# Kernel optimization log

Hardware: AMD Instinct MI355X
Metric: run time of the kernel (lower is better)

## Reference

```python
import jax, jax.numpy as jnp
import numpy as np

VOCAB, T, IN, H, L = 32000, 4096, 512, 256, 2


def setup_inputs() -> dict:
    key = jax.random.key(0)
    ks = jax.random.split(key, 32)
    inp = {}
    inp["tokens"] = jax.random.randint(ks[0], (T,), 0, VOCAB)
    inp["emb"] = jax.random.normal(ks[1], (VOCAB, IN), dtype=jnp.float32) * 0.02
    i = 2
    for d in ("f", "b"):
        for l in range(L):
            in_l = IN if l == 0 else H
            inp[f"{d}_Wih{l}"] = jax.random.normal(ks[i], (4 * H, in_l), dtype=jnp.float32) * 0.05; i += 1
            inp[f"{d}_Whh{l}"] = jax.random.normal(ks[i], (4 * H, H), dtype=jnp.float32) * 0.05; i += 1
            inp[f"{d}_bih{l}"] = jnp.zeros((4 * H,), dtype=jnp.float32)
            inp[f"{d}_bhh{l}"] = jnp.zeros((4 * H,), dtype=jnp.float32)
    return inp


def _lstm_layer(x_seq, Wih, Whh, bih, bhh):
    # x_seq: [T, in]; torch.nn.LSTMCell gate order: i, f, g, o
    Hh = Whh.shape[1]
    b = bih + bhh
    def step(carry, x):
        h, c = carry
        g = x @ Wih.T + h @ Whh.T + b           # [4H]
        i_, f_, g_, o_ = jnp.split(g, 4)
        c = jax.nn.sigmoid(f_) * c + jax.nn.sigmoid(i_) * jnp.tanh(g_)
        h = jax.nn.sigmoid(o_) * jnp.tanh(c)
        return (h, c), h
    z = jnp.zeros((Hh,), x_seq.dtype)
    (h, c), hs = jax.lax.scan(step, (z, z), x_seq)
    return hs, h, c                              # [T,H], [H], [H]


def _run_dir(x_seq, params):
    finals = []
    h_seq = x_seq
    for (Wih, Whh, bih, bhh) in params:
        h_seq, h, c = _lstm_layer(h_seq, Wih, Whh, bih, bhh)
        finals.append((c, h))
    return h_seq, finals


def reference(tokens, emb,
              f_Wih0, f_Whh0, f_bih0, f_bhh0, f_Wih1, f_Whh1, f_bih1, f_bhh1,
              b_Wih0, b_Whh0, b_bih0, b_bhh0, b_Wih1, b_Whh1, b_bih1, b_bhh1):
    x = emb[tokens]                              # [T, IN] embedding lookup
    fparams = [(f_Wih0, f_Whh0, f_bih0, f_bhh0), (f_Wih1, f_Whh1, f_bih1, f_bhh1)]
    bparams = [(b_Wih0, b_Whh0, b_bih0, b_bhh0), (b_Wih1, b_Whh1, b_bih1, b_bhh1)]
    f_out, f_fin = _run_dir(x, fparams)          # forward over sequence
    b_out_rev, b_fin = _run_dir(x[::-1], bparams)  # backward over reversed sequence
    b_out = b_out_rev[::-1]
    outputs = jnp.concatenate([f_out, b_out], axis=-1)  # [T, 2H]
    cell_memories = jnp.stack([jnp.stack([f_fin[l][0], b_fin[l][0]]) for l in range(L)])  # [L,2,H]
    hidden_states = jnp.stack([jnp.stack([f_fin[l][1], b_fin[l][1]]) for l in range(L)])  # [L,2,H]
    return cell_memories, hidden_states, outputs
```

## Files before the change

### kernel.cpp

```cpp
#include <hip/hip_runtime.h>
#include <math.h>

#define T_SEQ 4096

__device__ __forceinline__ float sigmoidf_(float x) {
  return 1.0f / (1.0f + expf(-x));
}

__device__ __forceinline__ unsigned long long pack_h(int tag, float h) {
  return ((unsigned long long)(unsigned)tag << 32) |
         (unsigned long long)__float_as_uint(h);
}

__device__ __forceinline__ unsigned long long ld_sc0(const unsigned long long* p) {
  unsigned long long v;
  asm volatile("global_load_dwordx2 %0, %1, off sc0\n\ts_waitcnt vmcnt(0)"
               : "=v"(v) : "v"(p) : "memory");
  return v;
}
__device__ __forceinline__ unsigned long long ld_mall(const unsigned long long* p) {
  unsigned long long v;
  asm volatile("global_load_dwordx2 %0, %1, off sc0 sc1\n\ts_waitcnt vmcnt(0)"
               : "=v"(v) : "v"(p) : "memory");
  return v;
}
__device__ __forceinline__ void st_pub(unsigned long long* p, unsigned long long v) {
  asm volatile("global_store_dwordx2 %0, %1, off sc0\n\t"
               "global_store_dwordx2 %0, %1, off sc0 sc1"
               :: "v"(p), "v"(v) : "memory");
}
__device__ __forceinline__ float poll_h(const unsigned long long* p, unsigned want) {
  int it = 0;
  for (;;) {
    unsigned long long v = ((it & 3) == 3) ? ld_mall(p) : ld_sc0(p);
    if ((unsigned)(v >> 32) == want) return __uint_as_float((unsigned)v);
    ++it;
  }
}

__global__ void gather_emb(const int* __restrict__ tokens,
                           const float4* __restrict__ emb4,
                           float4* __restrict__ X4) {
  int i = blockIdx.x * 256 + threadIdx.x;
  int t = i >> 7;
  int q = i & 127;
  X4[i] = emb4[(long)tokens[t] * 128 + q];
}

__global__ __launch_bounds__(256) void gemm_proj(
    const float* __restrict__ Xf, const float* __restrict__ Xb, int revb,
    const float* __restrict__ Wf, const float* __restrict__ Wb,
    const float* __restrict__ bihf, const float* __restrict__ bhhf,
    const float* __restrict__ bihb, const float* __restrict__ bhhb,
    float* __restrict__ Pf, float* __restrict__ Pb, int K)
{
  const int dirb = blockIdx.z;
  const float* X  = dirb ? Xb : Xf;
  const float* W  = dirb ? Wb : Wf;
  const float* bih = dirb ? bihb : bihf;
  const float* bhh = dirb ? bhhb : bhhf;
  float* Pp = dirb ? Pb : Pf;
  const int rev = dirb ? revb : 0;

  const int bn = blockIdx.x;
  const int bm = blockIdx.y;
  const int tid = threadIdx.x;
  const int tx = tid & 15, ty = tid >> 4;

  __shared__ float Xs[16][68];
  __shared__ float Ws[16][68];

  float acc[4][4] = {{0.f}};

  const int lrow = tid >> 2;
  const int lk4  = (tid & 3) * 4;
  const int xrow = bm * 64 + lrow;
  const int xsrc = rev ? (4095 - xrow) : xrow;
  const float* xptr = X + (long)xsrc * K + lk4;
  const float* wptr = W + (long)(bn * 64 + lrow) * K + lk4;

  for (int k0 = 0; k0 < K; k0 += 16) {
    float4 xv = *(const float4*)(xptr + k0);
    float4 wv = *(const float4*)(wptr + k0);
    __syncthreads();
    Xs[lk4 + 0][lrow] = xv.x; Xs[lk4 + 1][lrow] = xv.y;
    Xs[lk4 + 2][lrow] = xv.z; Xs[lk4 + 3][lrow] = xv.w;
    Ws[lk4 + 0][lrow] = wv.x; Ws[lk4 + 1][lrow] = wv.y;
    Ws[lk4 + 2][lrow] = wv.z; Ws[lk4 + 3][lrow] = wv.w;
    __syncthreads();
    #pragma unroll
    for (int kk = 0; kk < 16; ++kk) {
      float4 a = *(const float4*)(&Xs[kk][ty * 4]);
      float4 b = *(const float4*)(&Ws[kk][tx * 4]);
      acc[0][0] = fmaf(a.x, b.x, acc[0][0]); acc[0][1] = fmaf(a.x, b.y, acc[0][1]);
      acc[0][2] = fmaf(a.x, b.z, acc[0][2]); acc[0][3] = fmaf(a.x, b.w, acc[0][3]);
      acc[1][0] = fmaf(a.y, b.x, acc[1][0]); acc[1][1] = fmaf(a.y, b.y, acc[1][1]);
      acc[1][2] = fmaf(a.y, b.z, acc[1][2]); acc[1][3] = fmaf(a.y, b.w, acc[1][3]);
      acc[2][0] = fmaf(a.z, b.x, acc[2][0]); acc[2][1] = fmaf(a.z, b.y, acc[2][1]);
      acc[2][2] = fmaf(a.z, b.z, acc[2][2]); acc[2][3] = fmaf(a.z, b.w, acc[2][3]);
      acc[3][0] = fmaf(a.w, b.x, acc[3][0]); acc[3][1] = fmaf(a.w, b.y, acc[3][1]);
      acc[3][2] = fmaf(a.w, b.z, acc[3][2]); acc[3][3] = fmaf(a.w, b.w, acc[3][3]);
    }
  }

  const int c0 = bn * 64 + tx * 4;
  #pragma unroll
  for (int i = 0; i < 4; ++i) {
    const int r = bm * 64 + ty * 4 + i;
    float4 o4;
    o4.x = acc[i][0] + bih[c0 + 0] + bhh[c0 + 0];
    o4.y = acc[i][1] + bih[c0 + 1] + bhh[c0 + 1];
    o4.z = acc[i][2] + bih[c0 + 2] + bhh[c0 + 2];
    o4.w = acc[i][3] + bih[c0 + 3] + bhh[c0 + 3];
    *(float4*)(&Pp[(long)r * 1024 + c0]) = o4;
  }
}

__global__ __launch_bounds__(512, 2) void lstm_fused(
    const float* __restrict__ P0f, const float* __restrict__ P0b,
    const float* __restrict__ Whh0f, const float* __restrict__ Whh0b,
    const float* __restrict__ Wih1f, const float* __restrict__ Whh1f,
    const float* __restrict__ bih1f, const float* __restrict__ bhh1f,
    const float* __restrict__ Wih1b, const float* __restrict__ Whh1b,
    const float* __restrict__ bih1b, const float* __restrict__ bhh1b,
    float* __restrict__ out,
    unsigned long long* __restrict__ ring0,
    unsigned long long* __restrict__ h1x)
{
  const int bx = blockIdx.x;
  const int t  = threadIdx.x;

  const int lane8 = bx & 7;
  if (lane8 > 1) return;
  const int d   = lane8;
  const int sub = bx >> 3;

  __shared__ float hx[512];
  __shared__ float part[8 * 264];
  __shared__ float gact[256];
  __shared__ float lds_c[64];

  if (t < 64) lds_c[t] = 0.0f;

  unsigned long long* ring = ring0 + (long)d * T_SEQ * 256;

  if (sub < 4) {
    const int w = sub;
    const float* __restrict__ P = d ? P0b : P0f;
    const float* __restrict__ W = d ? Whh0b : Whh0f;

    const int kb = t >> 6;
    const int jg = t & 63;

    float wreg[128];
    #pragma unroll
    for (int jj = 0; jj < 4; ++jj) {
      const int m = jg * 4 + jj;
      const int j = (m >> 6) * 256 + w * 64 + (m & 63);
      const float4* wrow = (const float4*)(W + (long)j * 256 + kb * 32);
      #pragma unroll
      for (int kq = 0; kq < 8; ++kq) {
        float4 v = wrow[kq];
        wreg[jj * 32 + kq * 4 + 0] = v.x;
        wreg[jj * 32 + kq * 4 + 1] = v.y;
        wreg[jj * 32 + kq * 4 + 2] = v.z;
        wreg[jj * 32 + kq * 4 + 3] = v.w;
      }
    }

    const long pj   = (long)((t >> 6) * 256 + w * 64 + (t & 63));
    const int  cell = w * 64 + (t & 63);

    for (int s = 0; s < T_SEQ; ++s) {
      float pval = 0.0f;
      if (t < 256) pval = P[(long)s * 1024 + pj];

      if (s == 0) {
        if (t < 256) hx[t] = 0.0f;
      } else if (t < 256) {
        hx[t] = poll_h(ring + (long)(s - 1) * 256 + t, (unsigned)s);
      }
      __syncthreads();

      float a0 = 0.f, a1 = 0.f, a2 = 0.f, a3 = 0.f;
      const float4* h4 = (const float4*)&hx[kb * 32];
      #pragma unroll
      for (int kq = 0; kq < 8; ++kq) {
        float4 hv = h4[kq];
        a0 = fmaf(wreg[0 * 32 + kq * 4 + 0], hv.x, a0);
        a0 = fmaf(wreg[0 * 32 + kq * 4 + 1], hv.y, a0);
        a0 = fmaf(wreg[0 * 32 + kq * 4 + 2], hv.z, a0);
        a0 = fmaf(wreg[0 * 32 + kq * 4 + 3], hv.w, a0);
        a1 = fmaf(wreg[1 * 32 + kq * 4 + 0], hv.x, a1);
        a1 = fmaf(wreg[1 * 32 + kq * 4 + 1], hv.y, a1);
        a1 = fmaf(wreg[1 * 32 + kq * 4 + 2], hv.z, a1);
        a1 = fmaf(wreg[1 * 32 + kq * 4 + 3], hv.w, a1);
        a2 = fmaf(wreg[2 * 32 + kq * 4 + 0], hv.x, a2);
        a2 = fmaf(wreg[2 * 32 + kq * 4 + 1], hv.y, a2);
        a2 = fmaf(wreg[2 * 32 + kq * 4 + 2], hv.z, a2);
        a2 = fmaf(wreg[2 * 32 + kq * 4 + 3], hv.w, a2);
        a3 = fmaf(wreg[3 * 32 + kq * 4 + 0], hv.x, a3);
        a3 = fmaf(wreg[3 * 32 + kq * 4 + 1], hv.y, a3);
        a3 = fmaf(wreg[3 * 32 + kq * 4 + 2], hv.z, a3);
        a3 = fmaf(wreg[3 * 32 + kq * 4 + 3], hv.w, a3);
      }
      float4 av; av.x = a0; av.y = a1; av.z = a2; av.w = a3;
      *(float4*)(&part[kb * 264 + jg * 4]) = av;
      __syncthreads();

      if (t < 256) {
        float g = pval;
        #pragma unroll
        for (int q = 0; q < 8; ++q) g += part[q * 264 + t];
        gact[t] = ((t >> 6) == 2) ? tanhf(g) : sigmoidf_(g);
      }
      __syncthreads();

      if (t < 64) {
        float c = gact[64 + t] * lds_c[t] + gact[t] * gact[128 + t];
        float h = gact[192 + t] * tanhf(c);
        lds_c[t] = c;
        st_pub(ring + (long)s * 256 + cell, pack_h(s + 1, h));
        if (s == T_SEQ - 1) {
          out[d * 256 + cell] = c;
          out[1024 + d * 256 + cell] = h;
        }
      }
    }
  } else {
    const int w1 = sub - 4;
    const float* __restrict__ Wih = d ? Wih1b : Wih1f;
    const float* __restrict__ Whh = d ? Whh1b : Whh1f;
    const float* __restrict__ bih = d ? bih1b : bih1f;
    const float* __restrict__ bhh = d ? bhh1b : bhh1f;
    unsigned long long* slot = h1x + d * 512;
    float* hout = d ? (out + 2048 + (long)4095 * 512 + 256) : (out + 2048);
    const long hstr = d ? -512 : 512;

    const int kb = t >> 6;
    const int jg = t & 63;

    float wreg[2][64];
    #pragma unroll
    for (int rr = 0; rr < 2; ++rr) {
      const int m = jg * 2 + rr;
      const int j = (m >> 5) * 256 + w1 * 32 + (m & 31);
      const float* srcw = (kb < 4) ? (Wih + (long)j * 256 + kb * 64)
                                   : (Whh + (long)j * 256 + (kb - 4) * 64);
      const float4* s4 = (const float4*)srcw;
      #pragma unroll
      for (int q = 0; q < 16; ++q) {
        float4 v = s4[q];
        wreg[rr][q * 4 + 0] = v.x; wreg[rr][q * 4 + 1] = v.y;
        wreg[rr][q * 4 + 2] = v.z; wreg[rr][q * 4 + 3] = v.w;
      }
    }

    const int cell = w1 * 32 + (t & 31);
    float bsum = 0.0f;
    if (t < 128) {
      const int j = (t >> 5) * 256 + w1 * 32 + (t & 31);
      bsum = bih[j] + bhh[j];
    }

    for (int s = 0; s < T_SEQ; ++s) {
      if (t < 256) {
        hx[t] = poll_h(ring + (long)s * 256 + t, (unsigned)(s + 1));
      } else {
        hx[t] = poll_h(slot + ((s + 1) & 1) * 256 + (t - 256), (unsigned)s);
      }
      __syncthreads();

      float a0 = 0.f, a1 = 0.f;
      const float4* h4 = (const float4*)&hx[kb * 64];
      #pragma unroll
      for (int q = 0; q < 16; ++q) {
        float4 hv = h4[q];
        a0 = fmaf(wreg[0][q * 4 + 0], hv.x, a0);
        a0 = fmaf(wreg[0][q * 4 + 1], hv.y, a0);
        a0 = fmaf(wreg[0][q * 4 + 2], hv.z, a0);
        a0 = fmaf(wreg[0][q * 4 + 3], hv.w, a0);
        a1 = fmaf(wreg[1][q * 4 + 0], hv.x, a1);
        a1 = fmaf(wreg[1][q * 4 + 1], hv.y, a1);
        a1 = fmaf(wreg[1][q * 4 + 2], hv.z, a1);
        a1 = fmaf(wreg[1][q * 4 + 3], hv.w, a1);
      }
      float2 av2; av2.x = a0; av2.y = a1;
      *(float2*)(&part[kb * 264 + jg * 2]) = av2;
      __syncthreads();

      if (t < 128) {
        float g = bsum;
        #pragma unroll
        for (int q = 0; q < 8; ++q) g += part[q * 264 + t];
        gact[t] = ((t >> 5) == 2) ? tanhf(g) : sigmoidf_(g);
      }
      __syncthreads();

      if (t < 32) {
        float c = gact[32 + t] * lds_c[t] + gact[t] * gact[64 + t];
        float h = gact[96 + t] * tanhf(c);
        lds_c[t] = c;
        st_pub(&slot[(s & 1) * 256 + cell], pack_h(s + 1, h));
        hout[(long)s * hstr + cell] = h;
        if (s == T_SEQ - 1) {
          out[512 + d * 256 + cell] = c;
          out[1024 + 512 + d * 256 + cell] = h;
        }
      }
    }
  }
}

extern "C" void kernel_launch(void* const* d_in, const int* in_sizes, int n_in,
                              void* d_out, int out_size, void* d_ws, size_t ws_size,
                              hipStream_t stream) {
  const int*   tokens = (const int*)d_in[0];
  const float* emb    = (const float*)d_in[1];
  const float* fWih0 = (const float*)d_in[2];
  const float* fWhh0 = (const float*)d_in[3];
  const float* fbih0 = (const float*)d_in[4];
  const float* fbhh0 = (const float*)d_in[5];
  const float* fWih1 = (const float*)d_in[6];
  const float* fWhh1 = (const float*)d_in[7];
  const float* fbih1 = (const float*)d_in[8];
  const float* fbhh1 = (const float*)d_in[9];
  const float* bWih0 = (const float*)d_in[10];
  const float* bWhh0 = (const float*)d_in[11];
  const float* bbih0 = (const float*)d_in[12];
  const float* bbhh0 = (const float*)d_in[13];
  const float* bWih1 = (const float*)d_in[14];
  const float* bWhh1 = (const float*)d_in[15];
  const float* bbih1 = (const float*)d_in[16];
  const float* bbhh1 = (const float*)d_in[17];

  float* out = (float*)d_out;
  float* ws  = (float*)d_ws;

  float* X   = ws;
  float* P0f = ws + 4194304;
  float* P0b = ws + 8388608;
  unsigned long long* ring0 = (unsigned long long*)ws;
  unsigned long long* h1x   = (unsigned long long*)(ws + 12582912);

  gather_emb<<<2048, 256, 0, stream>>>(tokens, (const float4*)emb, (float4*)X);

  gemm_proj<<<dim3(16, 64, 2), 256, 0, stream>>>(
      X, X, 1, fWih0, bWih0, fbih0, fbhh0, bbih0, bbhh0, P0f, P0b, 512);

  hipMemsetAsync(ring0, 0, (size_t)2 * T_SEQ * 256 * sizeof(unsigned long long), stream);
  hipMemsetAsync(h1x, 0, 1024 * sizeof(unsigned long long), stream);

  lstm_fused<<<dim3(96), 512, 0, stream>>>(
      P0f, P0b, fWhh0, bWhh0,
      fWih1, fWhh1, fbih1, fbhh1,
      bWih1, bWhh1, bbih1, bbhh1,
      out, ring0, h1x);
}
```

Baseline: 7.324 ms.

## Write own hidden slice locally, prefetch projections, use lightweight barriers in LSTM loop

Each workgroup now writes its own freshly computed h cells straight into LDS and polls only the other groups' slices from the global ring, so part of the cross-workgroup wait is skipped. The input projection for the next step is prefetched one iteration ahead. __syncthreads is replaced by a custom barrier that waits only on LDS counters, the finishing threads are moved to the last wave, MALL polls are made less frequent, and launch bounds are relaxed to one block per CU. The custom barrier leaves global loads outstanding, which relies on the inline-asm polls waiting for themselves, and the looser launch bounds may change register allocation.

```diff
diff --git a/kernel.cpp b/kernel.cpp
--- a/kernel.cpp
+++ b/kernel.cpp
@@ -32,10 +32,16 @@
 __device__ __forceinline__ float poll_h(const unsigned long long* p, unsigned want) {
   int it = 0;
   for (;;) {
-    unsigned long long v = ((it & 3) == 3) ? ld_mall(p) : ld_sc0(p);
+    unsigned long long v = ((it & 7) == 7) ? ld_mall(p) : ld_sc0(p);
     if ((unsigned)(v >> 32) == want) return __uint_as_float((unsigned)v);
     ++it;
   }
+}
+
+__device__ __forceinline__ void bar() {
+  asm volatile("s_waitcnt lgkmcnt(0)" ::: "memory");
+  __builtin_amdgcn_s_barrier();
+  asm volatile("" ::: "memory");
 }
 
 __global__ void gather_emb(const int* __restrict__ tokens,
@@ -116,7 +122,7 @@
   }
 }
 
-__global__ __launch_bounds__(512, 2) void lstm_fused(
+__global__ __launch_bounds__(512, 1) void lstm_fused(
     const float* __restrict__ P0f, const float* __restrict__ P0b,
     const float* __restrict__ Whh0f, const float* __restrict__ Whh0b,
     const float* __restrict__ Wih1f, const float* __restrict__ Whh1f,
@@ -139,8 +145,6 @@
   __shared__ float part[8 * 264];
   __shared__ float gact[256];
   __shared__ float lds_c[64];
-
-  if (t < 64) lds_c[t] = 0.0f;
 
   unsigned long long* ring = ring0 + (long)d * T_SEQ * 256;
 
@@ -169,18 +173,22 @@
     }
 
     const long pj   = (long)((t >> 6) * 256 + w * 64 + (t & 63));
-    const int  cell = w * 64 + (t & 63);
+    const int ownlo = w * 64;
+    const int pcell = (t < ownlo) ? t : t + 64;
+    const int fidx  = t - 448;
+
+    float pv_cur = 0.0f;
+    if (t < 256) pv_cur = P[pj];
+    if (t < 256) hx[t] = 0.0f;
+    if (t >= 448) lds_c[fidx] = 0.0f;
 
     for (int s = 0; s < T_SEQ; ++s) {
-      float pval = 0.0f;
-      if (t < 256) pval = P[(long)s * 1024 + pj];
-
-      if (s == 0) {
-        if (t < 256) hx[t] = 0.0f;
-      } else if (t < 256) {
-        hx[t] = poll_h(ring + (long)(s - 1) * 256 + t, (unsigned)s);
-      }
-      __syncthreads();
+      if (s > 0 && t < 192) {
+        hx[pcell] = poll_h(ring + (long)(s - 1) * 256 + pcell, (unsigned)s);
+      }
+      float pv_next = 0.0f;
+      if (t < 256 && s + 1 < T_SEQ) pv_next = P[(long)(s + 1) * 1024 + pj];
+      bar();
 
       float a0 = 0.f, a1 = 0.f, a2 = 0.f, a3 = 0.f;
       const float4* h4 = (const float4*)&hx[kb * 32];
@@ -206,20 +214,23 @@
       }
       float4 av; av.x = a0; av.y = a1; av.z = a2; av.w = a3;
       *(float4*)(&part[kb * 264 + jg * 4]) = av;
-      __syncthreads();
+      bar();
 
       if (t < 256) {
-        float g = pval;
+        float g = pv_cur;
         #pragma unroll
         for (int q = 0; q < 8; ++q) g += part[q * 264 + t];
         gact[t] = ((t >> 6) == 2) ? tanhf(g) : sigmoidf_(g);
-      }
-      __syncthreads();
-
-      if (t < 64) {
-        float c = gact[64 + t] * lds_c[t] + gact[t] * gact[128 + t];
-        float h = gact[192 + t] * tanhf(c);
-        lds_c[t] = c;
+        pv_cur = pv_next;
+      }
+      bar();
+
+      if (t >= 448) {
+        const int cell = ownlo + fidx;
+        float c = gact[64 + fidx] * lds_c[fidx] + gact[fidx] * gact[128 + fidx];
+        float h = gact[192 + fidx] * tanhf(c);
+        lds_c[fidx] = c;
+        hx[cell] = h;
         st_pub(ring + (long)s * 256 + cell, pack_h(s + 1, h));
         if (s == T_SEQ - 1) {
           out[d * 256 + cell] = c;
@@ -256,20 +267,28 @@
       }
     }
 
-    const int cell = w1 * 32 + (t & 31);
+    const int fidx = t - 480;
+    const int t2   = t - 256;
+    const int pc1  = (t2 < w1 * 32) ? t2 : t2 + 32;
+
     float bsum = 0.0f;
     if (t < 128) {
       const int j = (t >> 5) * 256 + w1 * 32 + (t & 31);
       bsum = bih[j] + bhh[j];
     }
 
+    if (t >= 480) {
+      lds_c[fidx] = 0.0f;
+      hx[256 + w1 * 32 + fidx] = 0.0f;
+    }
+
     for (int s = 0; s < T_SEQ; ++s) {
       if (t < 256) {
         hx[t] = poll_h(ring + (long)s * 256 + t, (unsigned)(s + 1));
-      } else {
-        hx[t] = poll_h(slot + ((s + 1) & 1) * 256 + (t - 256), (unsigned)s);
-      }
-      __syncthreads();
+      } else if (t < 480) {
+        hx[256 + pc1] = poll_h(slot + ((s + 1) & 1) * 256 + pc1, (unsigned)s);
+      }
+      bar();
 
       float a0 = 0.f, a1 = 0.f;
       const float4* h4 = (const float4*)&hx[kb * 64];
@@ -287,7 +306,7 @@
       }
       float2 av2; av2.x = a0; av2.y = a1;
       *(float2*)(&part[kb * 264 + jg * 2]) = av2;
-      __syncthreads();
+      bar();
 
       if (t < 128) {
         float g = bsum;
@@ -295,12 +314,14 @@
         for (int q = 0; q < 8; ++q) g += part[q * 264 + t];
         gact[t] = ((t >> 5) == 2) ? tanhf(g) : sigmoidf_(g);
       }
-      __syncthreads();
-
-      if (t < 32) {
-        float c = gact[32 + t] * lds_c[t] + gact[t] * gact[64 + t];
-        float h = gact[96 + t] * tanhf(c);
-        lds_c[t] = c;
+      bar();
+
+      if (t >= 480) {
+        const int cell = w1 * 32 + fidx;
+        float c = gact[32 + fidx] * lds_c[fidx] + gact[fidx] * gact[64 + fidx];
+        float h = gact[96 + fidx] * tanhf(c);
+        lds_c[fidx] = c;
+        hx[256 + cell] = h;
         st_pub(&slot[(s & 1) * 256 + cell], pack_h(s + 1, h));
         hout[(long)s * hstr + cell] = h;
         if (s == T_SEQ - 1) {
```

After: 7.902 ms. +7.9%, slower.
